# Kernel tuning notes

Measured on AMD Instinct MI355X. Metric: run time of the kernel, lower is better.

The kernel has to match this reference:

```python
import jax, jax.numpy as jnp
import numpy as np

TOKENS, D_MODEL, FC1, FC2 = 4096, 4096, 16384, 4096
EPS = 1e-3


def setup_inputs() -> dict:
    key = jax.random.key(0)
    ks = jax.random.split(key, 3)
    return {
        "inputs": jax.random.normal(ks[0], (TOKENS, D_MODEL), dtype=jnp.float32),
        "gamma": jnp.ones((D_MODEL,), dtype=jnp.float32),
        "beta": jnp.zeros((D_MODEL,), dtype=jnp.float32),
        "fc1_kernel": jax.random.normal(ks[1], (D_MODEL, FC1), dtype=jnp.float32) * 0.023,
        "fc1_bias": jnp.zeros((FC1,), dtype=jnp.float32),
        "fc2_kernel": jax.random.normal(ks[2], (FC1, FC2), dtype=jnp.float32) * 0.023,
        "fc2_bias": jnp.zeros((FC2,), dtype=jnp.float32),
    }


def _layernorm(x, gamma, beta):
    mu = jnp.mean(x, axis=-1, keepdims=True)
    var = jnp.mean(jnp.square(x - mu), axis=-1, keepdims=True)
    rsigma = jax.lax.rsqrt(var + EPS)
    return (x - mu) * rsigma * gamma + beta


def _gelu_tanh(x):
    # gelu with approximate=True (tanh approximation)
    c = jnp.asarray(0.7978845608028654, x.dtype)  # sqrt(2/pi)
    return 0.5 * x * (1.0 + jnp.tanh(c * (x + 0.044715 * x * x * x)))


def reference(inputs, gamma, beta, fc1_kernel, fc1_bias, fc2_kernel, fc2_bias):
    ln_out = _layernorm(inputs, gamma, beta)            # [T, D]
    fc1_out = jnp.matmul(ln_out, fc1_kernel) + fc1_bias  # [T, FC1]
    gelu_out = _gelu_tanh(fc1_out)
    fc2_out = jnp.matmul(gelu_out, fc2_kernel) + fc2_bias  # [T, FC2]
    return fc2_out
```

## Files before the change

kernel.cpp:

```cpp
#include <hip/hip_runtime.h>
#include <stdint.h>

#define TOKENS 4096
#define DMODEL 4096
#define FC1N   16384
#define FC2N   4096

typedef __attribute__((ext_vector_type(8))) __bf16 bf16x8;
typedef __attribute__((ext_vector_type(4))) float f32x4;

__device__ __forceinline__ unsigned short f2bf(float f) {
  unsigned u = __float_as_uint(f);
  u += 0x7fffu + ((u >> 16) & 1u);
  return (unsigned short)(u >> 16);
}

__device__ __forceinline__ float gelu_tanh(float x) {
  float y = 0.7978845608028654f * (x + 0.044715f * x * x * x);
  float e = __expf(2.0f * y);
  float t = 1.0f - 2.0f / (e + 1.0f);
  return 0.5f * x * (1.0f + t);
}

__global__ __launch_bounds__(256) void ln_kernel(const float* __restrict__ x,
                                                 const float* __restrict__ gamma,
                                                 const float* __restrict__ beta,
                                                 unsigned short* __restrict__ out) {
  const int row = blockIdx.x;
  const int tid = threadIdx.x;
  const float* xr = x + (size_t)row * DMODEL;
  float4 v[4];
  float s = 0.f, s2 = 0.f;
#pragma unroll
  for (int i = 0; i < 4; ++i) {
    v[i] = ((const float4*)xr)[tid + i * 256];
    s  += v[i].x + v[i].y + v[i].z + v[i].w;
    s2 += v[i].x * v[i].x + v[i].y * v[i].y + v[i].z * v[i].z + v[i].w * v[i].w;
  }
#pragma unroll
  for (int o = 32; o > 0; o >>= 1) {
    s  += __shfl_xor(s, o, 64);
    s2 += __shfl_xor(s2, o, 64);
  }
  __shared__ float red[2][4];
  const int wid = tid >> 6, lane = tid & 63;
  if (lane == 0) { red[0][wid] = s; red[1][wid] = s2; }
  __syncthreads();
  s  = red[0][0] + red[0][1] + red[0][2] + red[0][3];
  s2 = red[1][0] + red[1][1] + red[1][2] + red[1][3];
  const float mu = s * (1.f / DMODEL);
  const float var = s2 * (1.f / DMODEL) - mu * mu;
  const float rs = rsqrtf(var + 1e-3f);
  unsigned short* orow = out + (size_t)row * DMODEL;
#pragma unroll
  for (int i = 0; i < 4; ++i) {
    const int c4 = tid + i * 256;
    float4 g = ((const float4*)gamma)[c4];
    float4 b = ((const float4*)beta)[c4];
    ushort4 o;
    o.x = f2bf((v[i].x - mu) * rs * g.x + b.x);
    o.y = f2bf((v[i].y - mu) * rs * g.y + b.y);
    o.z = f2bf((v[i].z - mu) * rs * g.z + b.z);
    o.w = f2bf((v[i].w - mu) * rs * g.w + b.w);
    ((ushort4*)orow)[c4] = o;
  }
}

__global__ __launch_bounds__(256) void transpose_bf16(const float* __restrict__ W,
                                                      unsigned short* __restrict__ Wt,
                                                      int K, int N) {
  __shared__ float t[32][33];
  const int x = threadIdx.x & 31, y = threadIdx.x >> 5;
  const int n0 = blockIdx.x << 5, k0 = blockIdx.y << 5;
#pragma unroll
  for (int i = 0; i < 4; ++i)
    t[y + i * 8][x] = W[(size_t)(k0 + y + i * 8) * N + n0 + x];
  __syncthreads();
#pragma unroll
  for (int i = 0; i < 4; ++i)
    Wt[(size_t)(n0 + y + i * 8) * K + k0 + x] = f2bf(t[x][y + i * 8]);
}


template <bool GELU>
__global__ __launch_bounds__(512, 2) void gemm256(const unsigned short* __restrict__ A,
                                                  const unsigned short* __restrict__ Bt,
                                                  const float* __restrict__ bias,
                                                  void* __restrict__ Cout,
                                                  int M, int N, int K) {
  extern __shared__ char smem[];
  const int tid = threadIdx.x;
  const int lane = tid & 63, wid = tid >> 6;
  const int lane15 = lane & 15, laneHi = lane >> 4;

  const int nwg = gridDim.x;
  const int bid = blockIdx.x;
  const int cpx = nwg >> 3;
  const int wg = (bid & 7) * cpx + (bid >> 3);
  const int nbx = N >> 8;
  const int bx = wg % nbx, by = wg / nbx;
  const int m0 = by << 8, n0 = bx << 8;
  const int wr = wid >> 2, wc = wid & 3;
  const int aRow0 = (wr << 7) + lane15;
  const int bRow0 = (wc << 6) + lane15;

  const int swz = (lane15 & 7) << 4;
  const int offA0 = aRow0 * 128 + ((laneHi << 4) ^ swz);
  const int offA1 = offA0 ^ 64;
  const int offB0 = 32768 + bRow0 * 128 + ((laneHi << 4) ^ swz);
  const int offB1 = offB0 ^ 64;

  const int o0 = tid << 4, o1 = (512 + tid) << 4;
  const int r0 = o0 >> 7, r1 = o1 >> 7;
  const size_t g0 = (size_t)r0 * (K * 2) + ((o0 & 127) ^ ((r0 & 7) << 4));
  const size_t g1 = (size_t)r1 * (K * 2) + ((o1 & 127) ^ ((r1 & 7) << 4));

  const char* pAlo = (const char*)(A  + (size_t)m0 * K);
  const char* pAhi = (const char*)(A  + (size_t)(m0 + 128) * K);
  const char* pBlo = (const char*)(Bt + (size_t)n0 * K);
  const char* pBhi = (const char*)(Bt + (size_t)(n0 + 128) * K);

  auto stage = [&](const char* panel, size_t ktb, int ldsoff) {
    __builtin_amdgcn_global_load_lds(
        (const __attribute__((address_space(1))) void*)(panel + ktb + g0),
        (__attribute__((address_space(3))) void*)(smem + ldsoff + o0), 16, 0, 0);
    __builtin_amdgcn_global_load_lds(
        (const __attribute__((address_space(1))) void*)(panel + ktb + g1),
        (__attribute__((address_space(3))) void*)(smem + ldsoff + o1), 16, 0, 0);
  };
  auto rd = [&](int off) -> bf16x8 { return *(const bf16x8*)(smem + off); };

  const int NT = K >> 6;
  const int NIT = NT >> 1;

  f32x4 acc[8][4];
#pragma unroll
  for (int m = 0; m < 8; ++m)
#pragma unroll
    for (int n = 0; n < 4; ++n) acc[m][n] = f32x4{0.f, 0.f, 0.f, 0.f};

  enum { B0_ALO = 0, B0_AHI = 16384, B0_BLO = 32768, B0_BHI = 49152,
         B1_ALO = 65536, B1_AHI = 81920, B1_BLO = 98304, B1_BHI = 114688 };

  stage(pBlo, 0, B0_BLO); stage(pBhi, 0, B0_BHI);
  stage(pAlo, 0, B0_ALO); stage(pAhi, 0, B0_AHI);
  stage(pBlo, 128, B1_BLO); stage(pBhi, 128, B1_BHI);
  stage(pAlo, 128, B1_ALO);
  asm volatile("s_waitcnt vmcnt(6)" ::: "memory");
  __builtin_amdgcn_sched_barrier(0);
  __builtin_amdgcn_s_barrier();
  __builtin_amdgcn_sched_barrier(0);

  bf16x8 aL[4][2], aH[4][2], bL[2][2], bH[2][2];

#define MFMA_Q(AF, BF, MO, NO)                                                   \
  __builtin_amdgcn_s_setprio(1);                                                 \
  _Pragma("unroll")                                                              \
  for (int ks = 0; ks < 2; ++ks)                                                 \
    _Pragma("unroll")                                                            \
    for (int m = 0; m < 4; ++m)                                                  \
      _Pragma("unroll")                                                          \
      for (int n = 0; n < 2; ++n)                                                \
        acc[m + MO][n + NO] = __builtin_amdgcn_mfma_f32_16x16x32_bf16(           \
            AF[m][ks], BF[n][ks], acc[m + MO][n + NO], 0, 0, 0);                 \
  __builtin_amdgcn_s_setprio(0);

  for (int it = 0; it < NIT; ++it) {
    const int u = it << 1;
    const size_t ktbV = (size_t)(u + 1) << 7;
    const int c2 = (u + 2 < NT) ? u + 2 : NT - 1;
    const int c3 = (u + 3 < NT) ? u + 3 : NT - 1;
    const size_t ktb2 = (size_t)c2 << 7, ktb3 = (size_t)c3 << 7;

#pragma unroll
    for (int m = 0; m < 4; ++m) {
      aL[m][0] = rd(offA0 + m * 2048); aL[m][1] = rd(offA1 + m * 2048);
    }
#pragma unroll
    for (int n = 0; n < 2; ++n) {
      bL[n][0] = rd(offB0 + n * 2048); bL[n][1] = rd(offB1 + n * 2048);
    }
    stage(pAhi, ktbV, B1_AHI);
    __builtin_amdgcn_s_barrier();
    MFMA_Q(aL, bL, 0, 0)
    __builtin_amdgcn_s_barrier();

#pragma unroll
    for (int n = 0; n < 2; ++n) {
      bH[n][0] = rd(offB0 + (n + 2) * 2048); bH[n][1] = rd(offB1 + (n + 2) * 2048);
    }
    __builtin_amdgcn_s_barrier();
    MFMA_Q(aL, bH, 0, 2)
    __builtin_amdgcn_s_barrier();

#pragma unroll
    for (int m = 0; m < 4; ++m) {
      aH[m][0] = rd(offA0 + (m + 4) * 2048); aH[m][1] = rd(offA1 + (m + 4) * 2048);
    }
    stage(pBlo, ktb2, B0_BLO); stage(pBhi, ktb2, B0_BHI);
    __builtin_amdgcn_s_barrier();
    MFMA_Q(aH, bH, 4, 2)
    __builtin_amdgcn_s_barrier();

    stage(pAlo, ktb2, B0_ALO);
    asm volatile("s_waitcnt vmcnt(6)" ::: "memory");
    __builtin_amdgcn_sched_barrier(0);
    __builtin_amdgcn_s_barrier();
    __builtin_amdgcn_sched_barrier(0);
    MFMA_Q(aH, bL, 4, 0)
    __builtin_amdgcn_s_barrier();

#pragma unroll
    for (int m = 0; m < 4; ++m) {
      aL[m][0] = rd(65536 + offA0 + m * 2048); aL[m][1] = rd(65536 + offA1 + m * 2048);
    }
#pragma unroll
    for (int n = 0; n < 2; ++n) {
      bL[n][0] = rd(65536 + offB0 + n * 2048); bL[n][1] = rd(65536 + offB1 + n * 2048);
    }
    stage(pAhi, ktb2, B0_AHI);
    __builtin_amdgcn_s_barrier();
    MFMA_Q(aL, bL, 0, 0)
    __builtin_amdgcn_s_barrier();

#pragma unroll
    for (int n = 0; n < 2; ++n) {
      bH[n][0] = rd(65536 + offB0 + (n + 2) * 2048);
      bH[n][1] = rd(65536 + offB1 + (n + 2) * 2048);
    }
    __builtin_amdgcn_s_barrier();
    MFMA_Q(aL, bH, 0, 2)
    __builtin_amdgcn_s_barrier();

#pragma unroll
    for (int m = 0; m < 4; ++m) {
      aH[m][0] = rd(65536 + offA0 + (m + 4) * 2048);
      aH[m][1] = rd(65536 + offA1 + (m + 4) * 2048);
    }
    stage(pBlo, ktb3, B1_BLO); stage(pBhi, ktb3, B1_BHI);
    __builtin_amdgcn_s_barrier();
    MFMA_Q(aH, bH, 4, 2)
    __builtin_amdgcn_s_barrier();

    stage(pAlo, ktb3, B1_ALO);
    asm volatile("s_waitcnt vmcnt(6)" ::: "memory");
    __builtin_amdgcn_sched_barrier(0);
    __builtin_amdgcn_s_barrier();
    __builtin_amdgcn_sched_barrier(0);
    MFMA_Q(aH, bL, 4, 0)
    __builtin_amdgcn_s_barrier();
  }
#undef MFMA_Q

#pragma unroll
  for (int nf = 0; nf < 4; ++nf) {
    const int col = n0 + (wc << 6) + (nf << 4) + lane15;
    const float bs = bias[col];
#pragma unroll
    for (int mf = 0; mf < 8; ++mf) {
      const int rbase = m0 + (wr << 7) + (mf << 4) + (laneHi << 2);
#pragma unroll
      for (int j = 0; j < 4; ++j) {
        const float v = acc[mf][nf][j] + bs;
        if (GELU) {
          ((unsigned short*)Cout)[(size_t)(rbase + j) * N + col] = f2bf(gelu_tanh(v));
        } else {
          ((float*)Cout)[(size_t)(rbase + j) * N + col] = v;
        }
      }
    }
  }
}

extern "C" void kernel_launch(void* const* d_in, const int* in_sizes, int n_in,
                              void* d_out, int out_size, void* d_ws, size_t ws_size,
                              hipStream_t stream) {
  const float* x     = (const float*)d_in[0];
  const float* gamma = (const float*)d_in[1];
  const float* beta  = (const float*)d_in[2];
  const float* w1    = (const float*)d_in[3];
  const float* b1    = (const float*)d_in[4];
  const float* w2    = (const float*)d_in[5];
  const float* b2    = (const float*)d_in[6];

  unsigned short* lnout = (unsigned short*)d_ws;
  unsigned short* gout  = (unsigned short*)((char*)d_ws + (size_t)32  * 1024 * 1024);
  unsigned short* wT    = (unsigned short*)((char*)d_ws + (size_t)160 * 1024 * 1024);

  (void)hipFuncSetAttribute((const void*)gemm256<true>,
                            hipFuncAttributeMaxDynamicSharedMemorySize, 131072);
  (void)hipFuncSetAttribute((const void*)gemm256<false>,
                            hipFuncAttributeMaxDynamicSharedMemorySize, 131072);

  ln_kernel<<<TOKENS, 256, 0, stream>>>(x, gamma, beta, lnout);

  transpose_bf16<<<dim3(FC1N / 32, DMODEL / 32), 256, 0, stream>>>(w1, wT, DMODEL, FC1N);
  gemm256<true><<<dim3((TOKENS / 256) * (FC1N / 256)), 512, 131072, stream>>>(
      lnout, wT, b1, (void*)gout, TOKENS, FC1N, DMODEL);

  transpose_bf16<<<dim3(FC2N / 32, FC1N / 32), 256, 0, stream>>>(w2, wT, FC1N, FC2N);
  gemm256<false><<<dim3((TOKENS / 256) * (FC2N / 256)), 512, 131072, stream>>>(
      gout, wT, b2, d_out, TOKENS, FC2N, FC1N);
}
```

Before: 1.146 ms.

## Reschedule GEMM ping-pong pipeline with finer-grained staged loads and waits

Restructures the double-buffered MFMA main loop so that each of the eight sub-phases issues one LDS fragment read and one global stage. The next buffer's B-low fragments are prefetched across iterations, and vmcnt waits are placed every two phases instead of once per half. Each MFMA block now waits on lgkmcnt(0) explicitly. The aim is to spread global loads and LDS reads evenly and overlap them better with matrix cores, at the cost of tighter hazard reasoning around buffer reuse.

```diff
diff --git a/kernel.cpp b/kernel.cpp
--- a/kernel.cpp
+++ b/kernel.cpp
@@ -145,15 +145,20 @@
   stage(pBlo, 0, B0_BLO); stage(pBhi, 0, B0_BHI);
   stage(pAlo, 0, B0_ALO); stage(pAhi, 0, B0_AHI);
   stage(pBlo, 128, B1_BLO); stage(pBhi, 128, B1_BHI);
-  stage(pAlo, 128, B1_ALO);
-  asm volatile("s_waitcnt vmcnt(6)" ::: "memory");
+  asm volatile("s_waitcnt vmcnt(4)" ::: "memory");
   __builtin_amdgcn_sched_barrier(0);
   __builtin_amdgcn_s_barrier();
   __builtin_amdgcn_sched_barrier(0);
 
   bf16x8 aL[4][2], aH[4][2], bL[2][2], bH[2][2];
 
+#pragma unroll
+  for (int n = 0; n < 2; ++n) {
+    bL[n][0] = rd(offB0 + n * 2048); bL[n][1] = rd(offB1 + n * 2048);
+  }
+
 #define MFMA_Q(AF, BF, MO, NO)                                                   \
+  asm volatile("s_waitcnt lgkmcnt(0)" ::: "memory");                             \
   __builtin_amdgcn_s_setprio(1);                                                 \
   _Pragma("unroll")                                                              \
   for (int ks = 0; ks < 2; ++ks)                                                 \
@@ -165,6 +170,34 @@
             AF[m][ks], BF[n][ks], acc[m + MO][n + NO], 0, 0, 0);                 \
   __builtin_amdgcn_s_setprio(0);
 
+#define RD_AL(B)                                                                 \
+  _Pragma("unroll")                                                              \
+  for (int m = 0; m < 4; ++m) {                                                  \
+    aL[m][0] = rd(B + offA0 + m * 2048); aL[m][1] = rd(B + offA1 + m * 2048);    \
+  }
+#define RD_AH(B)                                                                 \
+  _Pragma("unroll")                                                              \
+  for (int m = 0; m < 4; ++m) {                                                  \
+    aH[m][0] = rd(B + offA0 + (m + 4) * 2048);                                   \
+    aH[m][1] = rd(B + offA1 + (m + 4) * 2048);                                   \
+  }
+#define RD_BL(B)                                                                 \
+  _Pragma("unroll")                                                              \
+  for (int n = 0; n < 2; ++n) {                                                  \
+    bL[n][0] = rd(B + offB0 + n * 2048); bL[n][1] = rd(B + offB1 + n * 2048);    \
+  }
+#define RD_BH(B)                                                                 \
+  _Pragma("unroll")                                                              \
+  for (int n = 0; n < 2; ++n) {                                                  \
+    bH[n][0] = rd(B + offB0 + (n + 2) * 2048);                                   \
+    bH[n][1] = rd(B + offB1 + (n + 2) * 2048);                                   \
+  }
+#define BAR __builtin_amdgcn_s_barrier()
+#define SB  __builtin_amdgcn_sched_barrier(0)
+#define CHECK4                                                                   \
+  asm volatile("s_waitcnt vmcnt(4)" ::: "memory");                               \
+  SB;
+
   for (int it = 0; it < NIT; ++it) {
     const int u = it << 1;
     const size_t ktbV = (size_t)(u + 1) << 7;
@@ -172,85 +205,33 @@
     const int c3 = (u + 3 < NT) ? u + 3 : NT - 1;
     const size_t ktb2 = (size_t)c2 << 7, ktb3 = (size_t)c3 << 7;
 
-#pragma unroll
-    for (int m = 0; m < 4; ++m) {
-      aL[m][0] = rd(offA0 + m * 2048); aL[m][1] = rd(offA1 + m * 2048);
-    }
-#pragma unroll
-    for (int n = 0; n < 2; ++n) {
-      bL[n][0] = rd(offB0 + n * 2048); bL[n][1] = rd(offB1 + n * 2048);
-    }
-    stage(pAhi, ktbV, B1_AHI);
-    __builtin_amdgcn_s_barrier();
-    MFMA_Q(aL, bL, 0, 0)
-    __builtin_amdgcn_s_barrier();
-
-#pragma unroll
-    for (int n = 0; n < 2; ++n) {
-      bH[n][0] = rd(offB0 + (n + 2) * 2048); bH[n][1] = rd(offB1 + (n + 2) * 2048);
-    }
-    __builtin_amdgcn_s_barrier();
-    MFMA_Q(aL, bH, 0, 2)
-    __builtin_amdgcn_s_barrier();
-
-#pragma unroll
-    for (int m = 0; m < 4; ++m) {
-      aH[m][0] = rd(offA0 + (m + 4) * 2048); aH[m][1] = rd(offA1 + (m + 4) * 2048);
-    }
-    stage(pBlo, ktb2, B0_BLO); stage(pBhi, ktb2, B0_BHI);
-    __builtin_amdgcn_s_barrier();
-    MFMA_Q(aH, bH, 4, 2)
-    __builtin_amdgcn_s_barrier();
-
-    stage(pAlo, ktb2, B0_ALO);
-    asm volatile("s_waitcnt vmcnt(6)" ::: "memory");
-    __builtin_amdgcn_sched_barrier(0);
-    __builtin_amdgcn_s_barrier();
-    __builtin_amdgcn_sched_barrier(0);
-    MFMA_Q(aH, bL, 4, 0)
-    __builtin_amdgcn_s_barrier();
-
-#pragma unroll
-    for (int m = 0; m < 4; ++m) {
-      aL[m][0] = rd(65536 + offA0 + m * 2048); aL[m][1] = rd(65536 + offA1 + m * 2048);
-    }
-#pragma unroll
-    for (int n = 0; n < 2; ++n) {
-      bL[n][0] = rd(65536 + offB0 + n * 2048); bL[n][1] = rd(65536 + offB1 + n * 2048);
-    }
-    stage(pAhi, ktb2, B0_AHI);
-    __builtin_amdgcn_s_barrier();
-    MFMA_Q(aL, bL, 0, 0)
-    __builtin_amdgcn_s_barrier();
-
-#pragma unroll
-    for (int n = 0; n < 2; ++n) {
-      bH[n][0] = rd(65536 + offB0 + (n + 2) * 2048);
-      bH[n][1] = rd(65536 + offB1 + (n + 2) * 2048);
-    }
-    __builtin_amdgcn_s_barrier();
-    MFMA_Q(aL, bH, 0, 2)
-    __builtin_amdgcn_s_barrier();
-
-#pragma unroll
-    for (int m = 0; m < 4; ++m) {
-      aH[m][0] = rd(65536 + offA0 + (m + 4) * 2048);
-      aH[m][1] = rd(65536 + offA1 + (m + 4) * 2048);
-    }
-    stage(pBlo, ktb3, B1_BLO); stage(pBhi, ktb3, B1_BHI);
-    __builtin_amdgcn_s_barrier();
-    MFMA_Q(aH, bH, 4, 2)
-    __builtin_amdgcn_s_barrier();
-
-    stage(pAlo, ktb3, B1_ALO);
-    asm volatile("s_waitcnt vmcnt(6)" ::: "memory");
-    __builtin_amdgcn_sched_barrier(0);
-    __builtin_amdgcn_s_barrier();
-    __builtin_amdgcn_sched_barrier(0);
-    MFMA_Q(aH, bL, 4, 0)
-    __builtin_amdgcn_s_barrier();
+    RD_AL(0) stage(pAlo, ktbV, B1_ALO);
+    BAR; MFMA_Q(aL, bL, 0, 0) BAR;
+    RD_BH(0) stage(pAhi, ktbV, B1_AHI);
+    BAR; MFMA_Q(aL, bH, 0, 2) CHECK4 BAR; SB;
+    RD_AH(0) stage(pBlo, ktb2, B0_BLO);
+    BAR; MFMA_Q(aH, bL, 4, 0) BAR;
+    RD_BL(65536) stage(pBhi, ktb2, B0_BHI);
+    BAR; MFMA_Q(aH, bH, 4, 2) CHECK4 BAR; SB;
+    RD_AL(65536) stage(pAlo, ktb2, B0_ALO);
+    BAR; MFMA_Q(aL, bL, 0, 0) BAR;
+    RD_BH(65536) stage(pAhi, ktb2, B0_AHI);
+    BAR; MFMA_Q(aL, bH, 0, 2) CHECK4 BAR; SB;
+    RD_AH(65536) stage(pBlo, ktb3, B1_BLO);
+    BAR; MFMA_Q(aH, bL, 4, 0) BAR;
+    RD_BL(0) stage(pBhi, ktb3, B1_BHI);
+    BAR; MFMA_Q(aH, bH, 4, 2) CHECK4 BAR; SB;
   }
 #undef MFMA_Q
+#undef RD_AL
+#undef RD_AH
+#undef RD_BL
+#undef RD_BH
+#undef BAR
+#undef SB
+#undef CHECK4
+
+  asm volatile("s_waitcnt vmcnt(0)" ::: "memory");
 
 #pragma unroll
   for (int nf = 0; nf < 4; ++nf) {
```

Result: no change. 1.141 ms (-0.4%).
